# Performance work log

Hardware: AMD Instinct MI355X
Metric: run time of the kernel (lower is better)

The kernel has to match this reference:

```python
import jax, jax.numpy as jnp
import numpy as np

EPS = 1e-4
MP_SILU_C = 0.596
RES_T = 0.3
ATTN_T = 0.3
CLIP = 256.0
HEADS = 8


def normalize(x, dim, eps=EPS):
    # matches torch normalize: x / (eps + sqrt(norm.numel()/x.numel()) * ||x||_dim)
    norm = jnp.sqrt(jnp.sum(jnp.square(x.astype(jnp.float32)), axis=dim, keepdims=True))
    alpha = np.sqrt(norm.size / x.size)
    return x / (eps + alpha * norm).astype(x.dtype)


def mp_silu(x):
    return jax.nn.silu(x) / MP_SILU_C


def mp_sum(a, b, t):
    return (a * (1.0 - t) + b * t) / np.sqrt((1.0 - t) ** 2 + t ** 2)


def mp_conv(x, w, gain=1.0):
    # weight-normalized conv / linear (eval mode: no in-place weight copy)
    w = w.astype(jnp.float32)
    w = normalize(w, tuple(range(1, w.ndim)))
    fan = int(np.prod(w.shape[1:]))
    w = w * (gain / np.sqrt(fan))
    w = w.astype(x.dtype)
    if w.ndim == 2:
        return x @ w.T
    return jax.lax.conv_general_dilated(
        x, w, window_strides=(1, 1), padding='SAME',
        dimension_numbers=('NCHW', 'OIHW', 'NCHW'))


def setup_inputs() -> dict:
    key = jax.random.key(0)
    ks = jax.random.split(key, 8)
    return {
        'x': jax.random.normal(ks[0], (16, 256, 32, 32), jnp.float32),
        'emb': jax.random.normal(ks[1], (16, 1024), jnp.float32),
        'w_skip': jax.random.normal(ks[2], (512, 256, 1, 1), jnp.float32),
        'w_res0': jax.random.normal(ks[3], (512, 512, 3, 3), jnp.float32),
        'w_emb': jax.random.normal(ks[4], (512, 1024), jnp.float32),
        'w_res1': jax.random.normal(ks[5], (512, 512, 3, 3), jnp.float32),
        'w_qkv': jax.random.normal(ks[6], (1536, 512, 1, 1), jnp.float32),
        'w_proj': jax.random.normal(ks[7], (512, 512, 1, 1), jnp.float32),
        'emb_gain': jnp.zeros([], jnp.float32),
    }


def reference(x, emb, w_skip, w_res0, w_emb, w_res1, w_qkv, w_proj, emb_gain):
    # flavor='enc', resample_mode='keep'
    x = mp_conv(x, w_skip)          # conv_skip (in!=out)
    x = normalize(x, 1)             # pixel norm over channels
    y = mp_conv(mp_silu(x), w_res0)
    c = mp_conv(emb, w_emb, gain=emb_gain) + 1.0   # [N, C]
    y = mp_silu(y * c[:, :, None, None].astype(y.dtype))
    y = mp_conv(y, w_res1)
    x = mp_sum(x, y, RES_T)
    # QK-normalized self-attention over H*W tokens
    N, C, H, W = x.shape
    ch = C // HEADS
    y = mp_conv(x, w_qkv)                              # [N, 3C, H, W]
    y = y.reshape(N, HEADS, ch, 3, H * W)
    qkv = normalize(y, 2)                              # L2-normalize per-head channels
    q, k, v = qkv[:, :, :, 0, :], qkv[:, :, :, 1, :], qkv[:, :, :, 2, :]
    attn = jax.nn.softmax(
        jnp.einsum('nhcq,nhck->nhqk', q, k) / np.sqrt(ch), axis=3)
    y = jnp.einsum('nhqk,nhck->nhcq', attn, v).reshape(N, C, H, W)
    y = mp_conv(y, w_proj)
    x = mp_sum(x, y, ATTN_T)
    return jnp.clip(x, -CLIP, CLIP)
```

## Files before the change

### kernel.cpp

```cpp
#include <hip/hip_runtime.h>

typedef unsigned short u16;
typedef unsigned int   u32;
typedef __attribute__((ext_vector_type(8))) short bf16x8;
typedef __attribute__((ext_vector_type(4))) float f32x4;
typedef __attribute__((ext_vector_type(4))) int   int4v;

#define DEV static __device__ __forceinline__

DEV u16 f2b(float f){ u32 u = __builtin_bit_cast(u32,f); u = (u + 0x7FFFu + ((u>>16)&1u))>>16; return (u16)u; }
DEV float b2f(u16 h){ return __builtin_bit_cast(float,(u32)h<<16); }
DEV float mpsilu(float t){ return t/(1.f+__expf(-t)) * 1.6778523489932886f; }
DEV u32 cvtpk(float lo, float hi){ u32 r; asm("v_cvt_pk_bf16_f32 %0, %1, %2" : "=v"(r) : "v"(lo), "v"(hi)); return r; }

DEV void gload16(void* l, const void* g){
  __builtin_amdgcn_global_load_lds(
    (const __attribute__((address_space(1))) void*)g,
    (__attribute__((address_space(3))) void*)l, 16, 0, 0);
}

#define OFF_W0B    0ull
#define OFF_W1B    4718592ull
#define OFF_WSKIPB 9437184ull
#define OFF_WQKVB  9699328ull
#define OFF_WPROJB 11272192ull
#define OFF_WEMB   11796480ull
#define OFF_CEMB   13893632ull
#define OFF_XSKIP  13926400ull
#define OFF_YATT   13926400ull
#define OFF_XNORM  47480832ull
#define OFF_QKVRAW 47480832ull
#define OFF_PAD0   97812480ull
#define OFF_Q      97812480ull
#define OFF_PAD1   116752384ull
#define OFF_V      116752384ull
#define OFF_XB     135692288ull
#define OFF_XRESB  169246720ull
#define OFF_K      186023936ull

__global__ __launch_bounds__(256) void k_prep_weights(
    const float* __restrict__ w_skip, const float* __restrict__ w_res0,
    const float* __restrict__ w_emb,  const float* __restrict__ w_res1,
    const float* __restrict__ w_qkv,  const float* __restrict__ w_proj,
    const float* __restrict__ egain, char* __restrict__ ws)
{
  int b = blockIdx.x, tid = threadIdx.x, lane = tid&63, wid = tid>>6;
  const float* src; int fan, mode, o; u16* dstB=nullptr; float* dstF=nullptr; float gain=1.f;
  if(b<512)       { o=b;      src=w_res0+(size_t)o*4608; fan=4608; mode=1; dstB=(u16*)(ws+OFF_W0B); }
  else if(b<1024) { o=b-512;  src=w_res1+(size_t)o*4608; fan=4608; mode=1; dstB=(u16*)(ws+OFF_W1B); }
  else if(b<1536) { o=b-1024; src=w_skip+(size_t)o*256;  fan=256;  mode=0; dstB=(u16*)(ws+OFF_WSKIPB); }
  else if(b<3072) { o=b-1536; src=w_qkv+(size_t)o*512;   fan=512;  mode=0; dstB=(u16*)(ws+OFF_WQKVB); }
  else if(b<3584) { o=b-3072; src=w_proj+(size_t)o*512;  fan=512;  mode=0; dstB=(u16*)(ws+OFF_WPROJB); }
  else            { o=b-3584; src=w_emb+(size_t)o*1024;  fan=1024; mode=2; dstF=(float*)(ws+OFF_WEMB); gain=*egain; }
  float ss=0;
  for(int i=tid;i<fan;i+=256){ float v=src[i]; ss += v*v; }
  for(int i=1;i<64;i<<=1) ss += __shfl_xor(ss,i);
  __shared__ float red[4];
  if(lane==0) red[wid]=ss;
  __syncthreads();
  ss = red[0]+red[1]+red[2]+red[3];
  float scale = gain / (1e-4f*sqrtf((float)fan) + sqrtf(ss));
  for(int i=tid;i<fan;i+=256){
    float v = src[i]*scale;
    if(mode==0) dstB[(size_t)o*fan + i] = f2b(v);
    else if(mode==1){ int c=i/9, tap=i%9; dstB[(size_t)tap*262144 + o*512 + c] = f2b(v); }
    else dstF[(size_t)o*1024 + i] = v;
  }
}

__global__ __launch_bounds__(256) void k_zero_border(char* __restrict__ ws){
  int idx = blockIdx.x*256 + threadIdx.x;
  int4v z = {0,0,0,0};
  for(; idx < 270336; idx += 67584){
    int chunk = idx & 63;
    int rest  = idx >> 6;
    int bp    = rest % 132;
    int rest2 = rest / 132;
    int n     = rest2 & 15;
    int buf   = rest2 >> 4;
    int py, px;
    if(bp < 34){ py=0; px=bp; }
    else if(bp < 68){ py=33; px=bp-34; }
    else if(bp < 100){ py=1+(bp-68); px=0; }
    else { py=1+(bp-100); px=33; }
    char* dst = ws + OFF_PAD0 + (size_t)buf*18939904ull
              + ((size_t)n*1156 + (size_t)py*34 + px)*1024 + (chunk<<4);
    *(int4v*)dst = z;
  }
}

__global__ __launch_bounds__(256) void k_emb(const float* __restrict__ emb,
    const float* __restrict__ wembs, float* __restrict__ cemb)
{
  int gw = (blockIdx.x*256 + threadIdx.x)>>6, lane = threadIdx.x&63;
  int n = gw>>9, o = gw&511;
  const float* e = emb + (size_t)n*1024;
  const float* w = wembs + (size_t)o*1024;
  float s=0;
  for(int i=lane*4;i<1024;i+=256){
    float4 a=*(const float4*)(e+i), b=*(const float4*)(w+i);
    s += a.x*b.x + a.y*b.y + a.z*b.z + a.w*b.w;
  }
  for(int i=1;i<64;i<<=1) s += __shfl_xor(s,i);
  if(lane==0) cemb[n*512+o] = s + 1.0f;
}

__global__ __launch_bounds__(256) void k_cast_x(const float* __restrict__ x, u16* __restrict__ xb){
  __shared__ u16 t[64*257];
  int bid=blockIdx.x, tid=threadIdx.x;
  int n=bid>>4, p0=(bid&15)<<6;
  int p=tid&63, c0=tid>>6;
  for(int c=c0;c<256;c+=4)
    t[p*257+c] = f2b(x[((size_t)((n<<8)+c)<<10) + p0 + p]);
  __syncthreads();
  for(int task=tid;task<2048;task+=256){
    int pp=task>>5, oc=(task&31)<<3;
    union{u16 u[8]; int4v v;} pk;
    #pragma unroll
    for(int i=0;i<8;++i) pk.u[i]=t[pp*257+oc+i];
    *(int4v*)(xb + ((size_t)((n<<10)+p0+pp))*256 + oc) = pk.v;
  }
}

__global__ __launch_bounds__(512) void k_gemm(const u16* __restrict__ A, const u16* __restrict__ Bw,
    int K, int ntiles, int mode, u16* __restrict__ out_b,
    const u16* __restrict__ xresb, float* __restrict__ dout)
{
  __shared__ u16 SH[3*24576];
  int bid=blockIdx.x, tid=threadIdx.x;
  int cpx = gridDim.x>>3;
  bid = (bid&7)*cpx + (bid>>3);
  int per_n = ntiles<<2;
  int n = bid/per_n, rem = bid%per_n, mt = rem/ntiles, nt = rem%ntiles;
  int lane=tid&63, wid=tid>>6, lg=lane>>4, li=lane&15;
  int wm=(wid>>1)<<6, wn=(wid&1)<<6;
  f32x4 acc[4][4];
  f32x4 zz = {0.f,0.f,0.f,0.f};
  #pragma unroll
  for(int i=0;i<4;++i) for(int j=0;j<4;++j) acc[i][j]=zz;

  const char* apc = (const char*)(A + (size_t)(n*1024 + mt*256)*K);
  const char* bpc = (const char*)(Bw + (size_t)(nt*128)*K);
  int a_off[4], b_off[2], lofA[4], lofB[2];
  #pragma unroll
  for(int i=0;i<4;++i){
    int c = tid + (i<<9);
    int r = c>>3, sc = (c&7) ^ (r&7);
    lofA[i] = c<<4;
    a_off[i] = (r*K + sc*8)*2;
  }
  #pragma unroll
  for(int i=0;i<2;++i){
    int c = tid + (i<<9);
    int r = c>>3, sc = (c&7) ^ (r&7);
    lofB[i] = 32768 + (c<<4);
    b_off[i] = (r*K + sc*8)*2;
  }
  char* SB = (char*)SH;
  auto STAGE = [&](int step, int buf){
    int so = step<<7;
    char* base = SB + buf*49152;
    #pragma unroll
    for(int i=0;i<4;++i) gload16(base + lofA[i], apc + a_off[i] + so);
    #pragma unroll
    for(int i=0;i<2;++i) gload16(base + lofB[i], bpc + b_off[i] + so);
  };
  int nsteps = K>>6;
  STAGE(0,0); STAGE(1,1);
  int bufsel = 0;
  for(int t=0;t<nsteps;++t){
    if(t < nsteps-1){ asm volatile("s_waitcnt vmcnt(6)" ::: "memory"); }
    else            { asm volatile("s_waitcnt vmcnt(0)" ::: "memory"); }
    __builtin_amdgcn_s_barrier();
    __builtin_amdgcn_sched_barrier(0);
    if(t+2 < nsteps) STAGE(t+2, (t+2)%3);
    const char* Ab = SB + bufsel*49152;
    const char* Bb = Ab + 32768;
    #pragma unroll
    for(int ks=0;ks<2;++ks){
      bf16x8 a[4], b[4];
      int bo = (lg<<4) + (ks<<6);
      #pragma unroll
      for(int i=0;i<4;++i){ int r = wm + (i<<4) + li; a[i] = *(const bf16x8*)(Ab + r*128 + (bo ^ ((r&7)<<4))); }
      #pragma unroll
      for(int j=0;j<4;++j){ int r = wn + (j<<4) + li; b[j] = *(const bf16x8*)(Bb + r*128 + (bo ^ ((r&7)<<4))); }
      __builtin_amdgcn_s_setprio(1);
      #pragma unroll
      for(int i=0;i<4;++i)
        #pragma unroll
        for(int j=0;j<4;++j)
          acc[i][j] = __builtin_amdgcn_mfma_f32_16x16x32_bf16(a[i], b[j], acc[i][j], 0, 0, 0);
      __builtin_amdgcn_s_setprio(0);
    }
    bufsel = (bufsel==2) ? 0 : bufsel+1;
  }

  int N = ntiles<<7;
  #pragma unroll
  for(int mf=0;mf<4;++mf){
    #pragma unroll
    for(int nf=0;nf<4;++nf){
      int oc = nt*128 + wn + (nf<<4) + li;
      #pragma unroll
      for(int jj=0;jj<4;++jj){
        float v = acc[mf][nf][jj];
        int p = mt*256 + wm + (mf<<4) + (lg<<2) + jj;
        size_t idx = (size_t)(n*1024+p)*N + oc;
        if(mode==1) out_b[idx]=f2b(v);
        else{
          float xr = b2f(xresb[(size_t)(n*1024+p)*512 + oc]);
          float r = (xr*0.7f + v*0.3f)*1.3130643285972254f;
          r = fminf(fmaxf(r,-256.f),256.f);
          dout[((size_t)(n*512+oc)<<10) + p] = r;
        }
      }
    }
  }
}

__global__ __launch_bounds__(512) void k_conv3x3(const u16* __restrict__ inpad, const u16* __restrict__ wt,
    int mode, const float* __restrict__ cemb, const u16* __restrict__ xnormb,
    u16* __restrict__ ypad, u16* __restrict__ xresb)
{
  __shared__ char SB[147456];
  int bid=blockIdx.x, tid=threadIdx.x;
  bid = (bid&7)*32 + (bid>>3);
  int n=bid>>4, rem=bid&15, mt=rem>>2, nt=rem&3;
  int lane=tid&63, wid=tid>>6, lg=lane>>4, li=lane&15;
  int wm=(wid>>1)<<6, wn=(wid&1)<<6;
  int mt8 = mt<<3;
  f32x4 acc[4][4];
  f32x4 zz={0.f,0.f,0.f,0.f};
  #pragma unroll
  for(int i=0;i<4;++i) for(int j=0;j<4;++j) acc[i][j]=zz;

  const char* ipc = (const char*)(inpad + (size_t)n*591872);
  const char* wtc = (const char*)wt;
  int b_src[2], b_lds[2];
  #pragma unroll
  for(int i=0;i<2;++i){
    int c = tid + (i<<9);
    int r = c>>3, sc = (c&7) ^ (r&7);
    b_lds[i] = c<<4;
    b_src[i] = (nt*128+r)*1024 + sc*16;
  }
  int abase[4];
  #pragma unroll
  for(int i=0;i<4;++i){ int r = wm + (i<<4) + li; abase[i] = (r>>5)*34 + (r&31); }

  auto STAGE_B = [&](int tap, int kc, int buf){
    int off = tap*524288 + (kc<<7);
    char* base = SB + 98304 + buf*16384;
    #pragma unroll
    for(int i=0;i<2;++i) gload16(base + b_lds[i], wtc + b_src[i] + off);
  };
  auto STAGE_A = [&](int kcn){
    char* ad = SB + ((kcn&1)*49152);
    #pragma unroll
    for(int oo=0;oo<6;++oo){
      int o = wid + (oo<<3);
      int slot = (o<<3) + (lane>>3);
      if(slot > 339) slot = 339;
      int scol = ((lane&7)<<4) ^ ((slot&7)<<4);
      int py = (slot*241)>>13;
      int px = slot - py*34;
      gload16(ad + (o<<10) + ((lane)<<4),
              ipc + (size_t)((mt8+py)*34 + px)*1024 + (kcn<<7) + scol);
    }
  };

  STAGE_A(0);
  STAGE_B(0,0,0);
  STAGE_B(1,0,1);
  asm volatile("s_waitcnt vmcnt(2)" ::: "memory");
  __builtin_amdgcn_s_barrier();

  int t = 0, bufsel = 0;
  for(int kc=0;kc<8;++kc){
    const char* Ach = SB + ((kc&1)*49152);
    for(int tap=0;tap<9;++tap,++t){
      if(t>0){
        if(t==71)        { asm volatile("s_waitcnt vmcnt(0)" ::: "memory"); }
        else if(tap==8)  { asm volatile("s_waitcnt vmcnt(8)" ::: "memory"); }
        else             { asm volatile("s_waitcnt vmcnt(2)" ::: "memory"); }
        __builtin_amdgcn_s_barrier();
      }
      __builtin_amdgcn_sched_barrier(0);
      if(t+2 < 72){
        int tap2 = tap+2, kc2 = kc;
        if(tap2 >= 9){ tap2 -= 9; kc2++; }
        int sbuf = bufsel-1; if(sbuf<0) sbuf=2;
        STAGE_B(tap2, kc2, sbuf);
      }
      if(tap==7 && kc<7) STAGE_A(kc+1);
      int dy = (tap*11)>>5;
      int dd = dy*34 + (tap - dy*3);
      const char* Bb = SB + 98304 + bufsel*16384;
      #pragma unroll
      for(int ks=0;ks<2;++ks){
        bf16x8 a[4], b[4];
        int bo = (lg<<4) + (ks<<6);
        #pragma unroll
        for(int i=0;i<4;++i){
          int slot = abase[i] + dd;
          a[i] = *(const bf16x8*)(Ach + slot*128 + (bo ^ ((slot&7)<<4)));
        }
        #pragma unroll
        for(int j=0;j<4;++j){ int r = wn + (j<<4) + li; b[j] = *(const bf16x8*)(Bb + r*128 + (bo ^ ((r&7)<<4))); }
        __builtin_amdgcn_s_setprio(1);
        #pragma unroll
        for(int i=0;i<4;++i)
          #pragma unroll
          for(int j=0;j<4;++j)
            acc[i][j] = __builtin_amdgcn_mfma_f32_16x16x32_bf16(a[i], b[j], acc[i][j], 0, 0, 0);
        __builtin_amdgcn_s_setprio(0);
      }
      bufsel = (bufsel==2) ? 0 : bufsel+1;
    }
  }

  #pragma unroll
  for(int mf=0;mf<4;++mf){
    #pragma unroll
    for(int nf=0;nf<4;++nf){
      int oc = nt*128 + wn + (nf<<4) + li;
      float ce = (mode==0) ? cemb[n*512+oc] : 0.f;
      #pragma unroll
      for(int jj=0;jj<4;++jj){
        float v = acc[mf][nf][jj];
        int p = mt*256 + wm + (mf<<4) + (lg<<2) + jj;
        int py=p>>5, px=p&31;
        if(mode==0){
          float s = mpsilu(v*ce);
          ypad[((size_t)n*1156 + (size_t)(py+1)*34 + (px+1))*512 + oc] = f2b(s);
        }else{
          size_t ix = (size_t)(n*1024+p)*512 + oc;
          float r = (b2f(xnormb[ix])*0.7f + v*0.3f)*1.3130643285972254f;
          xresb[ix]=f2b(r);
        }
      }
    }
  }
}

__global__ __launch_bounds__(256) void k_pixnorm(const u16* __restrict__ xs,
    u16* __restrict__ xn, u16* __restrict__ pad0)
{
  int tid=threadIdx.x, lane=tid&63, wid=tid>>6;
  for(int p = blockIdx.x*4 + wid; p < 16384; p += gridDim.x*4){
    union{u16 u[8]; int4v v;} in;
    in.v = *(const int4v*)(xs + (size_t)p*512 + lane*8);
    float f[8]; float ss=0.f;
    #pragma unroll
    for(int i=0;i<8;++i){ f[i]=b2f(in.u[i]); ss += f[i]*f[i]; }
    for(int i=1;i<64;i<<=1) ss += __shfl_xor(ss,i);
    float sc = 1.f/(1e-4f + sqrtf(ss)*0.04419417382415922f);
    union{u16 u[8]; int4v v;} on, op;
    #pragma unroll
    for(int i=0;i<8;++i){ float v=f[i]*sc; on.u[i]=f2b(v); op.u[i]=f2b(mpsilu(v)); }
    *(int4v*)(xn + (size_t)p*512 + lane*8) = on.v;
    int n=p>>10, py=(p>>5)&31, px=p&31;
    u16* pd = pad0 + ((size_t)n*1156 + (size_t)(py+1)*34 + (px+1))*512;
    *(int4v*)(pd + lane*8) = op.v;
  }
}

__global__ __launch_bounds__(256) void k_qkv_norm(const u16* __restrict__ raw,
    u16* __restrict__ q, u16* __restrict__ k, u16* __restrict__ v)
{
  __shared__ u16 lraw[8*1536];
  __shared__ float lscale[192];
  int bid=blockIdx.x, tid=threadIdx.x;
  int n=bid>>7, p0=(bid&127)<<3;
  for(int cc=tid; cc<1536; cc+=256){
    int pix=cc/192, off=(cc%192)<<3;
    *(int4v*)(lraw + pix*1536 + off) = *(const int4v*)(raw + ((size_t)((n<<10)+p0+pix))*1536 + off);
  }
  __syncthreads();
  if(tid<192){
    int pix=tid/24, rem=tid%24, h=rem/3, w=rem%3;
    const u16* r = lraw + pix*1536 + h*192 + w;
    float ss=0;
    #pragma unroll
    for(int c=0;c<64;++c){ float f=b2f(r[c*3]); ss += f*f; }
    lscale[tid] = 1.f/(1e-4f + sqrtf(ss)*0.125f);
  }
  __syncthreads();
  for(int t=tid;t<512;t+=256){
    int pix=t>>6, h=(t>>3)&7, oct=(t&7)<<3;
    float sq=lscale[pix*24+h*3+0]*0.18033688011112043f;
    float sk=lscale[pix*24+h*3+1];
    const u16* r = lraw + pix*1536 + h*192;
    union{u16 u[8]; int4v vv;} pq, pk;
    #pragma unroll
    for(int i=0;i<8;++i){ int c=oct+i; pq.u[i]=f2b(b2f(r[3*c+0])*sq); pk.u[i]=f2b(b2f(r[3*c+1])*sk); }
    size_t base = ((size_t)((n<<3)+h)<<10) + p0 + pix;
    *(int4v*)(q + base*64 + oct) = pq.vv;
    *(int4v*)(k + base*64 + oct) = pk.vv;
  }
  for(int t=tid;t<512;t+=256){
    int h=t>>6, c=t&63;
    union{u16 u[8]; int4v vv;} pv;
    #pragma unroll
    for(int pix=0;pix<8;++pix)
      pv.u[pix] = f2b(b2f(lraw[pix*1536 + h*192 + 3*c + 2]) * lscale[pix*24+h*3+2]);
    *(int4v*)(v + (((size_t)((n<<3)+h)<<6) + c)*1024 + p0) = pv.vv;
  }
}

__global__ __launch_bounds__(256) void k_attn(const u16* __restrict__ Q, const u16* __restrict__ Kb,
    const u16* __restrict__ Vb, u16* __restrict__ yatt)
{
  __shared__ char lds[49152];
  __shared__ float alds[4][32];
  int bid=blockIdx.x, tid=threadIdx.x;
  int pair = (bid&7)*16 + (bid>>6);
  int qt = (bid>>3)&7;
  int n=pair>>3, h=pair&7;
  const char* qb = (const char*)(Q  + ((size_t)pair*1024 + qt*128)*64);
  const char* kb = (const char*)(Kb + (size_t)pair*1024*64);
  const char* vb = (const char*)(Vb + (size_t)pair*64*1024);
  int lane=tid&63, wid=tid>>6, lg=lane>>4, li=lane&15;
  int wq=wid<<5;
  char* Pt = lds + 32768;

  #pragma unroll
  for(int i=0;i<4;++i){
    int c = lane + (i<<6);
    int r = wq + (c>>3);
    int sc = ((c&7) ^ (r&7))<<4;
    gload16(Pt + (wq<<7) + (c<<4), qb + (size_t)r*128 + sc);
  }
  asm volatile("s_waitcnt vmcnt(0)" ::: "memory");
  bf16x8 bq[2][2];
  #pragma unroll
  for(int qq=0;qq<2;++qq)
    #pragma unroll
    for(int ks=0;ks<2;++ks){
      int r=wq+(qq<<4)+li; int bo=(lg<<4)+(ks<<6);
      bq[qq][ks]=*(const bf16x8*)(Pt + r*128 + (bo ^ ((r&7)<<4)));
    }
  asm volatile("s_waitcnt lgkmcnt(0)" ::: "memory");
  __builtin_amdgcn_sched_barrier(0);

  auto STAGE = [&](int kt, int buf){
    char* kd = lds + buf*16384;
    #pragma unroll
    for(int i=0;i<2;++i){
      int c = tid + (i<<8);
      int r = c>>3;
      int sc = ((c&7) ^ (r&7))<<4;
      gload16(kd + (c<<4), kb + (size_t)kt*8192 + (r<<7) + sc);
    }
    #pragma unroll
    for(int i=0;i<2;++i){
      int c = tid + (i<<8);
      int r = c>>3;
      int sc = ((c&7) ^ (r&7))<<4;
      gload16(kd + 8192 + (c<<4), vb + (size_t)r*2048 + kt*128 + sc);
    }
  };
  STAGE(0,0);

  f32x4 o0[2][4];
  float m0=-1e30f, m1=-1e30f, l0=0.f, l1=0.f;
  f32x4 zz={0.f,0.f,0.f,0.f};
  #pragma unroll
  for(int i=0;i<2;++i) for(int j=0;j<4;++j) o0[i][j]=zz;

  for(int kt=0;kt<16;++kt){
    asm volatile("s_waitcnt vmcnt(0)" ::: "memory");
    __builtin_amdgcn_s_barrier();
    __builtin_amdgcn_sched_barrier(0);
    if(kt<15) STAGE(kt+1, (kt+1)&1);
    const char* Kt = lds + (kt&1)*16384;
    const char* Vt = Kt + 8192;
    f32x4 s[4][2];
    #pragma unroll
    for(int i=0;i<4;++i){ s[i][0]=zz; s[i][1]=zz; }
    #pragma unroll
    for(int ks=0;ks<2;++ks){
      int bo=(lg<<4)+(ks<<6);
      bf16x8 a[4];
      #pragma unroll
      for(int kk=0;kk<4;++kk){ int r=(kk<<4)+li; a[kk]=*(const bf16x8*)(Kt + r*128 + (bo ^ ((r&7)<<4))); }
      __builtin_amdgcn_s_setprio(1);
      #pragma unroll
      for(int kk=0;kk<4;++kk)
        #pragma unroll
        for(int qq=0;qq<2;++qq)
          s[kk][qq] = __builtin_amdgcn_mfma_f32_16x16x32_bf16(a[kk], bq[qq][ks], s[kk][qq], 0,0,0);
      __builtin_amdgcn_s_setprio(0);
    }
    float pm0=-1e30f, pm1=-1e30f;
    #pragma unroll
    for(int kk=0;kk<4;++kk)
      #pragma unroll
      for(int jj=0;jj<4;++jj){ pm0=fmaxf(pm0,s[kk][0][jj]); pm1=fmaxf(pm1,s[kk][1][jj]); }
    pm0=fmaxf(pm0,__shfl_xor(pm0,16)); pm0=fmaxf(pm0,__shfl_xor(pm0,32));
    pm1=fmaxf(pm1,__shfl_xor(pm1,16)); pm1=fmaxf(pm1,__shfl_xor(pm1,32));
    if(!__all((pm0 <= m0+11.5f) && (pm1 <= m1+11.5f))){
      float mn0=fmaxf(m0,pm0), mn1=fmaxf(m1,pm1);
      float al0=__builtin_amdgcn_exp2f(m0-mn0), al1=__builtin_amdgcn_exp2f(m1-mn1);
      if(lg==0){ alds[wid][li]=al0; alds[wid][16+li]=al1; }
      m0=mn0; m1=mn1; l0*=al0; l1*=al1;
      #pragma unroll
      for(int mf=0;mf<2;++mf)
        #pragma unroll
        for(int jj=0;jj<4;++jj){
          float am = alds[wid][(mf<<4)+(lg<<2)+jj];
          #pragma unroll
          for(int cf=0;cf<4;++cf) o0[mf][cf][jj]*=am;
        }
    }
    float rs0=0.f, rs1=0.f;
    #pragma unroll
    for(int kk=0;kk<4;++kk)
      #pragma unroll
      for(int jj=0;jj<4;++jj){
        float p0=__builtin_amdgcn_exp2f(s[kk][0][jj]-m0); s[kk][0][jj]=p0; rs0+=p0;
        float p1=__builtin_amdgcn_exp2f(s[kk][1][jj]-m1); s[kk][1][jj]=p1; rs1+=p1;
      }
    rs0+=__shfl_xor(rs0,16); rs0+=__shfl_xor(rs0,32);
    rs1+=__shfl_xor(rs1,16); rs1+=__shfl_xor(rs1,32);
    l0+=rs0; l1+=rs1;
    #pragma unroll
    for(int qq=0;qq<2;++qq){
      int q = wq+(qq<<4)+li;
      int rsw = (q&7)<<4;
      #pragma unroll
      for(int kk=0;kk<4;++kk){
        uint2 w;
        w.x = cvtpk(s[kk][qq][0], s[kk][qq][1]);
        w.y = cvtpk(s[kk][qq][2], s[kk][qq][3]);
        int bo = ((kk<<5)+(lg<<3)) ^ rsw;
        *(uint2*)(Pt + q*128 + bo) = w;
      }
    }
    #pragma unroll
    for(int ks=0;ks<2;++ks){
      int bo=(lg<<4)+(ks<<6);
      bf16x8 a[2], b[4];
      #pragma unroll
      for(int i=0;i<2;++i){ int r=wq+(i<<4)+li; a[i]=*(const bf16x8*)(Pt + r*128 + (bo ^ ((r&7)<<4))); }
      #pragma unroll
      for(int j=0;j<4;++j){ int r=(j<<4)+li;    b[j]=*(const bf16x8*)(Vt + r*128 + (bo ^ ((r&7)<<4))); }
      __builtin_amdgcn_s_setprio(1);
      #pragma unroll
      for(int i=0;i<2;++i)
        #pragma unroll
        for(int j=0;j<4;++j)
          o0[i][j] = __builtin_amdgcn_mfma_f32_16x16x32_bf16(a[i], b[j], o0[i][j], 0,0,0);
      __builtin_amdgcn_s_setprio(0);
    }
  }
  if(lg==0){ alds[wid][li]=1.f/l0; alds[wid][16+li]=1.f/l1; }
  #pragma unroll
  for(int mf=0;mf<2;++mf)
    #pragma unroll
    for(int jj=0;jj<4;++jj){
      float rl = alds[wid][(mf<<4)+(lg<<2)+jj];
      int p=(qt<<7)+wq+(mf<<4)+(lg<<2)+jj;
      #pragma unroll
      for(int nf=0;nf<4;++nf){
        int c=(nf<<4)+li;
        yatt[((size_t)(n*1024)+p)*512 + (h<<6) + c] = f2b(o0[mf][nf][jj]*rl);
      }
    }
}

extern "C" void kernel_launch(void* const* d_in, const int* in_sizes, int n_in,
                              void* d_out, int out_size, void* d_ws, size_t ws_size,
                              hipStream_t stream)
{
  (void)in_sizes; (void)n_in; (void)out_size; (void)ws_size;
  const float* x      = (const float*)d_in[0];
  const float* emb    = (const float*)d_in[1];
  const float* w_skip = (const float*)d_in[2];
  const float* w_res0 = (const float*)d_in[3];
  const float* w_emb  = (const float*)d_in[4];
  const float* w_res1 = (const float*)d_in[5];
  const float* w_qkv  = (const float*)d_in[6];
  const float* w_proj = (const float*)d_in[7];
  const float* egain  = (const float*)d_in[8];
  char* ws = (char*)d_ws;
  float* dout = (float*)d_out;

  u16* w0b    = (u16*)(ws+OFF_W0B);
  u16* w1b    = (u16*)(ws+OFF_W1B);
  u16* wskipb = (u16*)(ws+OFF_WSKIPB);
  u16* wqkvb  = (u16*)(ws+OFF_WQKVB);
  u16* wprojb = (u16*)(ws+OFF_WPROJB);
  float* wembs= (float*)(ws+OFF_WEMB);
  float* cemb = (float*)(ws+OFF_CEMB);
  u16* xskipb = (u16*)(ws+OFF_XSKIP);
  u16* yatt   = (u16*)(ws+OFF_YATT);
  u16* xnormb = (u16*)(ws+OFF_XNORM);
  u16* qkvraw = (u16*)(ws+OFF_QKVRAW);
  u16* pad0   = (u16*)(ws+OFF_PAD0);
  u16* qbuf   = (u16*)(ws+OFF_Q);
  u16* pad1   = (u16*)(ws+OFF_PAD1);
  u16* vbuf   = (u16*)(ws+OFF_V);
  u16* xb     = (u16*)(ws+OFF_XB);
  u16* xresb  = (u16*)(ws+OFF_XRESB);
  u16* kbuf   = (u16*)(ws+OFF_K);

  hipLaunchKernelGGL(k_prep_weights, dim3(4096), dim3(256), 0, stream,
                     w_skip, w_res0, w_emb, w_res1, w_qkv, w_proj, egain, ws);
  hipLaunchKernelGGL(k_zero_border, dim3(264), dim3(256), 0, stream, ws);
  hipLaunchKernelGGL(k_emb, dim3(2048), dim3(256), 0, stream, emb, wembs, cemb);
  hipLaunchKernelGGL(k_cast_x, dim3(256), dim3(256), 0, stream, x, xb);
  hipLaunchKernelGGL(k_gemm, dim3(256), dim3(512), 0, stream,
                     xb, wskipb, 256, 4, 1, xskipb, (const u16*)nullptr, (float*)nullptr);
  hipLaunchKernelGGL(k_pixnorm, dim3(1024), dim3(256), 0, stream, xskipb, xnormb, pad0);
  hipLaunchKernelGGL(k_conv3x3, dim3(256), dim3(512), 0, stream,
                     pad0, w0b, 0, cemb, (const u16*)nullptr, pad1, (u16*)nullptr);
  hipLaunchKernelGGL(k_conv3x3, dim3(256), dim3(512), 0, stream,
                     pad1, w1b, 1, (const float*)nullptr, xnormb, (u16*)nullptr, xresb);
  hipLaunchKernelGGL(k_gemm, dim3(768), dim3(512), 0, stream,
                     xresb, wqkvb, 512, 12, 1, qkvraw, (const u16*)nullptr, (float*)nullptr);
  hipLaunchKernelGGL(k_qkv_norm, dim3(2048), dim3(256), 0, stream, qkvraw, qbuf, kbuf, vbuf);
  hipLaunchKernelGGL(k_attn, dim3(1024), dim3(256), 0, stream, qbuf, kbuf, vbuf, yatt);
  hipLaunchKernelGGL(k_gemm, dim3(256), dim3(512), 0, stream,
                     yatt, wprojb, 512, 4, 2, (u16*)nullptr, xresb, dout);
}
```

Measured before the change: 399.6 us.

## Restructure 3x3 conv to 4 waves with 128x64 warp tiles and simpler pipeline

The 3x3 conv kernel drops from 512 to 256 threads. Each wave now computes a 128x64 output tile with 8x4 MFMA accumulators instead of 4x4, which doubles register reuse of B fragments. The A tile is single-buffered, B goes from triple to double buffering, and LDS use falls from 144KB to 76KB. The cost is that A is no longer prefetched: the next input channel chunk now loads behind a barrier at each kc boundary, and the larger accumulator set raises register pressure.

```diff
diff --git a/kernel.cpp b/kernel.cpp
--- a/kernel.cpp
+++ b/kernel.cpp
@@ -218,109 +218,99 @@
   }
 }
 
-__global__ __launch_bounds__(512) void k_conv3x3(const u16* __restrict__ inpad, const u16* __restrict__ wt,
+__global__ __launch_bounds__(256) void k_conv3x3(const u16* __restrict__ inpad, const u16* __restrict__ wt,
     int mode, const float* __restrict__ cemb, const u16* __restrict__ xnormb,
     u16* __restrict__ ypad, u16* __restrict__ xresb)
 {
-  __shared__ char SB[147456];
+  __shared__ char SB[77824];
   int bid=blockIdx.x, tid=threadIdx.x;
   bid = (bid&7)*32 + (bid>>3);
   int n=bid>>4, rem=bid&15, mt=rem>>2, nt=rem&3;
   int lane=tid&63, wid=tid>>6, lg=lane>>4, li=lane&15;
-  int wm=(wid>>1)<<6, wn=(wid&1)<<6;
+  int wm=(wid>>1)<<7, wn=(wid&1)<<6;
   int mt8 = mt<<3;
-  f32x4 acc[4][4];
+  f32x4 acc[8][4];
   f32x4 zz={0.f,0.f,0.f,0.f};
   #pragma unroll
-  for(int i=0;i<4;++i) for(int j=0;j<4;++j) acc[i][j]=zz;
+  for(int i=0;i<8;++i)
+    #pragma unroll
+    for(int j=0;j<4;++j) acc[i][j]=zz;
 
   const char* ipc = (const char*)(inpad + (size_t)n*591872);
   const char* wtc = (const char*)wt;
-  int b_src[2], b_lds[2];
-  #pragma unroll
-  for(int i=0;i<2;++i){
-    int c = tid + (i<<9);
-    int r = c>>3, sc = (c&7) ^ (r&7);
-    b_lds[i] = c<<4;
-    b_src[i] = (nt*128+r)*1024 + sc*16;
-  }
-  int abase[4];
-  #pragma unroll
-  for(int i=0;i<4;++i){ int r = wm + (i<<4) + li; abase[i] = (r>>5)*34 + (r&31); }
+  int abase[8];
+  #pragma unroll
+  for(int i=0;i<8;++i){ int r = wm + (i<<4) + li; abase[i] = (r>>5)*34 + (r&31); }
 
   auto STAGE_B = [&](int tap, int kc, int buf){
     int off = tap*524288 + (kc<<7);
-    char* base = SB + 98304 + buf*16384;
-    #pragma unroll
-    for(int i=0;i<2;++i) gload16(base + b_lds[i], wtc + b_src[i] + off);
+    char* base = SB + 45056 + buf*16384;
+    #pragma unroll
+    for(int i=0;i<4;++i){
+      int c = tid + (i<<8);
+      int r = c>>3, sc = ((c&7) ^ (r&7))<<4;
+      gload16(base + (c<<4), wtc + (nt*128+r)*1024 + sc + off);
+    }
   };
   auto STAGE_A = [&](int kcn){
-    char* ad = SB + ((kcn&1)*49152);
-    #pragma unroll
-    for(int oo=0;oo<6;++oo){
-      int o = wid + (oo<<3);
-      int slot = (o<<3) + (lane>>3);
-      if(slot > 339) slot = 339;
-      int scol = ((lane&7)<<4) ^ ((slot&7)<<4);
+    #pragma unroll
+    for(int i=0;i<11;++i){
+      int c = tid + (i<<8);
+      int slot = c>>3; if(slot>339) slot=339;
+      int scol = ((c&7) ^ (slot&7))<<4;
       int py = (slot*241)>>13;
       int px = slot - py*34;
-      gload16(ad + (o<<10) + ((lane)<<4),
-              ipc + (size_t)((mt8+py)*34 + px)*1024 + (kcn<<7) + scol);
+      gload16(SB + (c<<4), ipc + (size_t)((mt8+py)*34+px)*1024 + (kcn<<7) + scol);
     }
   };
 
   STAGE_A(0);
   STAGE_B(0,0,0);
-  STAGE_B(1,0,1);
-  asm volatile("s_waitcnt vmcnt(2)" ::: "memory");
+  asm volatile("s_waitcnt vmcnt(0)" ::: "memory");
   __builtin_amdgcn_s_barrier();
 
-  int t = 0, bufsel = 0;
+  int bbuf = 0;
   for(int kc=0;kc<8;++kc){
-    const char* Ach = SB + ((kc&1)*49152);
-    for(int tap=0;tap<9;++tap,++t){
-      if(t>0){
-        if(t==71)        { asm volatile("s_waitcnt vmcnt(0)" ::: "memory"); }
-        else if(tap==8)  { asm volatile("s_waitcnt vmcnt(8)" ::: "memory"); }
-        else             { asm volatile("s_waitcnt vmcnt(2)" ::: "memory"); }
-        __builtin_amdgcn_s_barrier();
-      }
+    for(int tap=0;tap<9;++tap){
+      if(tap<8){ STAGE_B(tap+1, kc, bbuf^1);
+                 asm volatile("s_waitcnt vmcnt(4)" ::: "memory"); }
+      else     { asm volatile("s_waitcnt vmcnt(0)" ::: "memory"); }
+      __builtin_amdgcn_s_barrier();
       __builtin_amdgcn_sched_barrier(0);
-      if(t+2 < 72){
-        int tap2 = tap+2, kc2 = kc;
-        if(tap2 >= 9){ tap2 -= 9; kc2++; }
-        int sbuf = bufsel-1; if(sbuf<0) sbuf=2;
-        STAGE_B(tap2, kc2, sbuf);
-      }
-      if(tap==7 && kc<7) STAGE_A(kc+1);
       int dy = (tap*11)>>5;
       int dd = dy*34 + (tap - dy*3);
-      const char* Bb = SB + 98304 + bufsel*16384;
+      const char* Bb = SB + 45056 + bbuf*16384;
       #pragma unroll
       for(int ks=0;ks<2;++ks){
-        bf16x8 a[4], b[4];
+        bf16x8 a[8], b[4];
         int bo = (lg<<4) + (ks<<6);
         #pragma unroll
-        for(int i=0;i<4;++i){
+        for(int i=0;i<8;++i){
           int slot = abase[i] + dd;
-          a[i] = *(const bf16x8*)(Ach + slot*128 + (bo ^ ((slot&7)<<4)));
+          a[i] = *(const bf16x8*)(SB + slot*128 + (bo ^ ((slot&7)<<4)));
         }
         #pragma unroll
         for(int j=0;j<4;++j){ int r = wn + (j<<4) + li; b[j] = *(const bf16x8*)(Bb + r*128 + (bo ^ ((r&7)<<4))); }
         __builtin_amdgcn_s_setprio(1);
         #pragma unroll
-        for(int i=0;i<4;++i)
+        for(int i=0;i<8;++i)
           #pragma unroll
           for(int j=0;j<4;++j)
             acc[i][j] = __builtin_amdgcn_mfma_f32_16x16x32_bf16(a[i], b[j], acc[i][j], 0, 0, 0);
         __builtin_amdgcn_s_setprio(0);
       }
-      bufsel = (bufsel==2) ? 0 : bufsel+1;
-    }
-  }
-
-  #pragma unroll
-  for(int mf=0;mf<4;++mf){
+      if(tap<8) bbuf ^= 1;
+    }
+    if(kc<7){
+      __builtin_amdgcn_s_barrier();
+      STAGE_A(kc+1);
+      STAGE_B(0, kc+1, bbuf^1);
+      bbuf ^= 1;
+    }
+  }
+
+  #pragma unroll
+  for(int mf=0;mf<8;++mf){
     #pragma unroll
     for(int nf=0;nf<4;++nf){
       int oc = nt*128 + wn + (nf<<4) + li;
@@ -613,9 +603,9 @@
   hipLaunchKernelGGL(k_gemm, dim3(256), dim3(512), 0, stream,
                      xb, wskipb, 256, 4, 1, xskipb, (const u16*)nullptr, (float*)nullptr);
   hipLaunchKernelGGL(k_pixnorm, dim3(1024), dim3(256), 0, stream, xskipb, xnormb, pad0);
-  hipLaunchKernelGGL(k_conv3x3, dim3(256), dim3(512), 0, stream,
+  hipLaunchKernelGGL(k_conv3x3, dim3(256), dim3(256), 0, stream,
                      pad0, w0b, 0, cemb, (const u16*)nullptr, pad1, (u16*)nullptr);
-  hipLaunchKernelGGL(k_conv3x3, dim3(256), dim3(512), 0, stream,
+  hipLaunchKernelGGL(k_conv3x3, dim3(256), dim3(256), 0, stream,
                      pad1, w1b, 1, (const float*)nullptr, xnormb, (u16*)nullptr, xresb);
   hipLaunchKernelGGL(k_gemm, dim3(768), dim3(512), 0, stream,
                      xresb, wqkvb, 512, 12, 1, qkvraw, (const u16*)nullptr, (float*)nullptr);
```

Result: slower. 431.0 us (+7.9%).
